# Optimization experiments

Hardware: AMD Instinct MI355X
Metric: run time of the kernel (lower is better)

The kernel has to match this reference:

```python
import jax, jax.numpy as jnp
import numpy as np

B, S, D_MODEL = 2, 2048, 1024
HEADS = 16
DK = D_MODEL // HEADS  # 64
Q_RANK, RANK = 6, 2
ROPE_BASE = 10000.0


def _xavier(key, shape):
    # torch nn.init.xavier_uniform_ on weight (out,in); stored here as (in,out)
    fan_in, fan_out = shape
    a = (6.0 / (fan_in + fan_out)) ** 0.5
    return jax.random.uniform(key, shape, jnp.float32, -a, a)


def setup_inputs() -> dict:
    key = jax.random.key(0)
    ks = jax.random.split(key, 10)
    inp = {
        "q": jax.random.normal(ks[0], (B, S, D_MODEL), jnp.float32),
        "k": jax.random.normal(ks[1], (B, S, D_MODEL), jnp.float32),
        "v": jax.random.normal(ks[2], (B, S, D_MODEL), jnp.float32),
        # causal mask; mask==0 -> -inf in scores
        "mask": jnp.tril(jnp.ones((S, S), dtype=bool))[None, None],
        "W_Aq": _xavier(ks[3], (D_MODEL, Q_RANK * HEADS)),
        "W_Ak": _xavier(ks[4], (D_MODEL, RANK * HEADS)),
        "W_Av": _xavier(ks[5], (D_MODEL, RANK * HEADS)),
        "W_Bq": _xavier(ks[6], (D_MODEL, Q_RANK * DK)),
        "W_Bk": _xavier(ks[7], (D_MODEL, RANK * DK)),
        "W_Bv": _xavier(ks[8], (D_MODEL, RANK * DK)),
        "Wo": _xavier(ks[9], (D_MODEL, D_MODEL)),
    }
    return inp


def _rotary_cos_sin(seq_len, dim):
    inv_freq = 1.0 / (ROPE_BASE ** (jnp.arange(0, dim, 2, dtype=jnp.float32) / dim))
    freqs = jnp.outer(jnp.arange(seq_len, dtype=jnp.float32), inv_freq)  # [S, dim/2]
    return jnp.cos(freqs)[None, :, None, :], jnp.sin(freqs)[None, :, None, :]


def _apply_rotary(x, cos, sin):
    # x: [B, S, R, dk]; rotate-half style RoPE
    d = x.shape[-1] // 2
    x1, x2 = x[..., :d], x[..., d:]
    return jnp.concatenate([x1 * cos + x2 * sin, -x1 * sin + x2 * cos], axis=-1)


def reference(q, k, v, mask, W_Aq, W_Ak, W_Av, W_Bq, W_Bk, W_Bv, Wo):
    Bn, Sn, D = q.shape
    # low-rank factor projections
    A_q = (q @ W_Aq).reshape(Bn, Sn, HEADS, Q_RANK)
    A_k = (k @ W_Ak).reshape(Bn, Sn, HEADS, RANK)
    A_v = (v @ W_Av).reshape(Bn, Sn, HEADS, RANK)
    B_q = (q @ W_Bq).reshape(Bn, Sn, Q_RANK, DK)
    B_k = (k @ W_Bk).reshape(Bn, Sn, RANK, DK)
    B_v = (v @ W_Bv).reshape(Bn, Sn, RANK, DK)
    cos, sin = _rotary_cos_sin(Sn, DK)
    B_q = _apply_rotary(B_q, cos, sin)
    B_k = _apply_rotary(B_k, cos, sin)
    # reconstruct per-head q/k/v: [B,H,S,dk]
    qh = jnp.einsum("bshr,bsrd->bhsd", A_q, B_q) / Q_RANK
    kh = jnp.einsum("bshr,bsrd->bhsd", A_k, B_k) / RANK
    vh = jnp.einsum("bshr,bsrd->bhsd", A_v, B_v) / RANK
    # NOTE: original divides by d_k (not sqrt(d_k)) -- faithful to source
    score = jnp.einsum("bhqd,bhkd->bhqk", qh, kh) / DK
    score = jnp.where(mask, score, -jnp.inf)
    # dropout is identity (eval / dropout=0.0)
    att = jax.nn.softmax(score, axis=-1)
    out = jnp.einsum("bhqk,bhkd->bqhd", att, vh).reshape(Bn, Sn, D)
    return out @ Wo
```

## Files before the change

### kernel.cpp

```cpp
#include <hip/hip_runtime.h>
#include <hip/hip_bf16.h>


typedef __attribute__((ext_vector_type(8))) short short8;
typedef __attribute__((ext_vector_type(4))) float floatx4;

#define MFMA16(a, b, c) __builtin_amdgcn_mfma_f32_16x16x32_bf16(a, b, c, 0, 0, 0)

__global__ __launch_bounds__(256) void cast3_kernel(const float* __restrict__ q,
                                                    const float* __restrict__ k,
                                                    const float* __restrict__ v,
                                                    __hip_bfloat16* __restrict__ qb,
                                                    __hip_bfloat16* __restrict__ kb,
                                                    __hip_bfloat16* __restrict__ vb) {
    const float* in = blockIdx.y == 0 ? q : blockIdx.y == 1 ? k : v;
    __hip_bfloat16* out = blockIdx.y == 0 ? qb : blockIdx.y == 1 ? kb : vb;
    int i = (blockIdx.x * 256 + threadIdx.x) * 4;
    float4 val = *(const float4*)(in + i);
    out[i + 0] = __float2bfloat16(val.x);
    out[i + 1] = __float2bfloat16(val.y);
    out[i + 2] = __float2bfloat16(val.z);
    out[i + 3] = __float2bfloat16(val.w);
}

__device__ __forceinline__ float wsrc(int n, int k,
                                      const float* __restrict__ Aq, const float* __restrict__ Bq,
                                      const float* __restrict__ Ak, const float* __restrict__ Bk,
                                      const float* __restrict__ Av, const float* __restrict__ Bv,
                                      const float* __restrict__ Wo) {
    if (n < 96) return Aq[(size_t)k * 96 + n];
    if (n < 480) return Bq[(size_t)k * 384 + (n - 96)];
    if (n < 512) return 0.f;
    if (n < 544) return Ak[(size_t)k * 32 + (n - 512)];
    if (n < 672) return Bk[(size_t)k * 128 + (n - 544)];
    if (n < 768) return 0.f;
    if (n < 800) return Av[(size_t)k * 32 + (n - 768)];
    if (n < 928) return Bv[(size_t)k * 128 + (n - 800)];
    if (n < 1024) return 0.f;
    return Wo[(size_t)k * 1024 + (n - 1024)];
}

__global__ __launch_bounds__(256) void pack_wT_kernel(const float* __restrict__ Aq,
                                                      const float* __restrict__ Bq,
                                                      const float* __restrict__ Ak,
                                                      const float* __restrict__ Bk,
                                                      const float* __restrict__ Av,
                                                      const float* __restrict__ Bv,
                                                      const float* __restrict__ Wo,
                                                      __hip_bfloat16* __restrict__ outBase) {
    __shared__ float tile[64][65];
    int k0 = blockIdx.x * 64, n0 = blockIdx.y * 64;
    int tid = threadIdx.x;
#pragma unroll
    for (int p = 0; p < 16; ++p) {
        int idx = p * 256 + tid;
        int kl = idx >> 6, nl = idx & 63;
        tile[kl][nl] = wsrc(n0 + nl, k0 + kl, Aq, Bq, Ak, Bk, Av, Bv, Wo);
    }
    __syncthreads();
#pragma unroll
    for (int p = 0; p < 16; ++p) {
        int idx = p * 256 + tid;
        int nl = idx >> 6, kl = idx & 63;
        outBase[(size_t)(n0 + nl) * 1024 + k0 + kl] = __float2bfloat16(tile[kl][nl]);
    }
}

__device__ __forceinline__ void gemm_body(const __hip_bfloat16* __restrict__ A,
                                          const __hip_bfloat16* __restrict__ BT,
                                          float* __restrict__ C, int N, int K,
                                          int m0, int n0) {
    __shared__ __align__(16) __hip_bfloat16 As[128][72];
    __shared__ __align__(16) __hip_bfloat16 Bs[128][72];
    int tid = threadIdx.x;
    int wave = tid >> 6, lane = tid & 63, quad = lane >> 4, l15 = lane & 15;
    int wm = wave >> 1, wn = wave & 1;
    floatx4 acc[4][4];
#pragma unroll
    for (int mt = 0; mt < 4; ++mt)
#pragma unroll
        for (int nt = 0; nt < 4; ++nt) acc[mt][nt] = (floatx4){0.f, 0.f, 0.f, 0.f};

    for (int k0 = 0; k0 < K; k0 += 64) {
#pragma unroll
        for (int p = 0; p < 4; ++p) {
            int idx = p * 256 + tid;
            int row = idx >> 3, c8 = (idx & 7) * 8;
            *(uint4*)&As[row][c8] = *(const uint4*)(A + (size_t)(m0 + row) * K + k0 + c8);
            *(uint4*)&Bs[row][c8] = *(const uint4*)(BT + (size_t)(n0 + row) * K + k0 + c8);
        }
        __syncthreads();
#pragma unroll
        for (int ks = 0; ks < 64; ks += 32) {
            short8 af[4], bf[4];
#pragma unroll
            for (int t = 0; t < 4; ++t) {
                af[t] = *(const short8*)&As[wm * 64 + t * 16 + l15][ks + quad * 8];
                bf[t] = *(const short8*)&Bs[wn * 64 + t * 16 + l15][ks + quad * 8];
            }
#pragma unroll
            for (int mt = 0; mt < 4; ++mt)
#pragma unroll
                for (int nt = 0; nt < 4; ++nt)
                    acc[mt][nt] = MFMA16(af[mt], bf[nt], acc[mt][nt]);
        }
        __syncthreads();
    }
#pragma unroll
    for (int mt = 0; mt < 4; ++mt)
#pragma unroll
        for (int nt = 0; nt < 4; ++nt)
#pragma unroll
            for (int r = 0; r < 4; ++r) {
                int row = m0 + wm * 64 + mt * 16 + quad * 4 + r;
                int col = n0 + wn * 64 + nt * 16 + l15;
                C[(size_t)row * N + col] = acc[mt][nt][r];
            }
}

__global__ __launch_bounds__(256) void gemm_bf16_kernel(const __hip_bfloat16* __restrict__ A,
                                                        const __hip_bfloat16* __restrict__ BT,
                                                        float* __restrict__ C, int N, int K) {
    gemm_body(A, BT, C, N, K, blockIdx.y * 128, blockIdx.x * 128);
}

__global__ __launch_bounds__(256) void gemm3_kernel(const __hip_bfloat16* __restrict__ qb,
                                                    const __hip_bfloat16* __restrict__ kb,
                                                    const __hip_bfloat16* __restrict__ vb,
                                                    const __hip_bfloat16* __restrict__ WqT,
                                                    const __hip_bfloat16* __restrict__ WkT,
                                                    const __hip_bfloat16* __restrict__ WvT,
                                                    float* __restrict__ Pq,
                                                    float* __restrict__ Pk,
                                                    float* __restrict__ Pv) {
    int t = blockIdx.x;
    const __hip_bfloat16* A; const __hip_bfloat16* BT; float* C; int N, nb;
    if (t < 4)      { A = qb; BT = WqT; C = Pq; N = 512; nb = t; }
    else if (t < 6) { A = kb; BT = WkT; C = Pk; N = 256; nb = t - 4; }
    else            { A = vb; BT = WvT; C = Pv; N = 256; nb = t - 6; }
    gemm_body(A, BT, C, N, 1024, blockIdx.y * 128, nb * 128);
}

__global__ __launch_bounds__(256) void combine_rope_kernel(const float* __restrict__ Pq,
                                                           const float* __restrict__ Pk,
                                                           const float* __restrict__ Pv,
                                                           __hip_bfloat16* __restrict__ qh,
                                                           __hip_bfloat16* __restrict__ kh,
                                                           __hip_bfloat16* __restrict__ vh) {
    int t = blockIdx.x, tid = threadIdx.x;
    int b = t >> 11, s = t & 2047;
    __shared__ float Lq[512], Lk[256], Lv[256];
    for (int i = tid; i < 512; i += 256) Lq[i] = Pq[(size_t)t * 512 + i];
    Lk[tid] = Pk[(size_t)t * 256 + tid];
    Lv[tid] = Pv[(size_t)t * 256 + tid];
    __syncthreads();
    if (tid < 192) {
        int r = tid >> 5, d = tid & 31;
        float inv = expf(-(float)d * 0.28782313662425576f);
        float sn, cs;
        sincosf((float)s * inv, &sn, &cs);
        float x1 = Lq[96 + r * 64 + d], x2 = Lq[96 + r * 64 + d + 32];
        Lq[96 + r * 64 + d] = x1 * cs + x2 * sn;
        Lq[96 + r * 64 + d + 32] = -x1 * sn + x2 * cs;
    } else {
        int i2 = tid - 192;
        int r = i2 >> 5, d = i2 & 31;
        float inv = expf(-(float)d * 0.28782313662425576f);
        float sn, cs;
        sincosf((float)s * inv, &sn, &cs);
        float x1 = Lk[32 + r * 64 + d], x2 = Lk[32 + r * 64 + d + 32];
        Lk[32 + r * 64 + d] = x1 * cs + x2 * sn;
        Lk[32 + r * 64 + d + 32] = -x1 * sn + x2 * cs;
    }
    __syncthreads();
    const float QSCALE = 1.4426950408889634f / 768.0f;
    int bh0 = b * 16;
    for (int i = tid; i < 1024; i += 256) {
        int h = i >> 6, d = i & 63;
        float aq = 0.f;
#pragma unroll
        for (int r = 0; r < 6; ++r) aq += Lq[h * 6 + r] * Lq[96 + r * 64 + d];
        size_t o = ((size_t)(bh0 + h) * 2048 + s) * 64 + d;
        qh[o] = __float2bfloat16(aq * QSCALE);
        float ak = Lk[h * 2] * Lk[32 + d] + Lk[h * 2 + 1] * Lk[96 + d];
        kh[o] = __float2bfloat16(ak);
        float av = Lv[h * 2] * Lv[32 + d] + Lv[h * 2 + 1] * Lv[96 + d];
        vh[o] = __float2bfloat16(av * 0.5f);
    }
}

__global__ __launch_bounds__(256) void transpose_v_kernel(const __hip_bfloat16* __restrict__ vh,
                                                          __hip_bfloat16* __restrict__ vT) {
    __shared__ __hip_bfloat16 tile[64][65];
    int s0 = blockIdx.x * 64, bh = blockIdx.y;
    int tid = threadIdx.x;
#pragma unroll
    for (int p = 0; p < 16; ++p) {
        int idx = p * 256 + tid;
        int r = idx >> 6, c = idx & 63;
        tile[r][c] = vh[((size_t)bh * 2048 + s0 + r) * 64 + c];
    }
    __syncthreads();
#pragma unroll
    for (int p = 0; p < 16; ++p) {
        int idx = p * 256 + tid;
        int r = idx >> 6, c = idx & 63;
        vT[((size_t)bh * 64 + r) * 2048 + s0 + c] = tile[c][r];
    }
}

__global__ __launch_bounds__(256) void flash_kernel(const __hip_bfloat16* __restrict__ qh,
                                                    const __hip_bfloat16* __restrict__ kh,
                                                    const __hip_bfloat16* __restrict__ vT,
                                                    __hip_bfloat16* __restrict__ att) {
    int lin = blockIdx.x + (blockIdx.y << 5);
    int bh = ((lin & 7) << 2) | ((lin >> 3) & 3);
    int qi = 31 - (lin >> 5);
    int tid = threadIdx.x;
    int wave = tid >> 6, lane = tid & 63, quad = lane >> 4, l15 = lane & 15;
    int q0 = qi * 64;
    __shared__ __align__(16) __hip_bfloat16 Ks[64][72];
    __shared__ __align__(16) __hip_bfloat16 Vts[64][72];
    __shared__ __align__(16) __hip_bfloat16 Ps[4][16][72];

    const __hip_bfloat16* qrow = qh + ((size_t)bh * 2048 + q0 + wave * 16 + l15) * 64 + quad * 8;
    short8 aq0 = *(const short8*)(qrow);
    short8 aq1 = *(const short8*)(qrow + 32);

    floatx4 o[4];
#pragma unroll
    for (int nt = 0; nt < 4; ++nt) o[nt] = (floatx4){0.f, 0.f, 0.f, 0.f};
    float rs[4] = {0.f, 0.f, 0.f, 0.f};

    for (int j = 0; j <= qi; ++j) {
        int k0 = j * 64;
#pragma unroll
        for (int p = 0; p < 2; ++p) {
            int idx = p * 256 + tid;
            int row = idx >> 3, c8 = (idx & 7) * 8;
            *(uint4*)&Ks[row][c8] = *(const uint4*)(kh + ((size_t)bh * 2048 + k0 + row) * 64 + c8);
            *(uint4*)&Vts[row][c8] = *(const uint4*)(vT + ((size_t)bh * 64 + row) * 2048 + k0 + c8);
        }
        __syncthreads();

        floatx4 s[4];
#pragma unroll
        for (int nt = 0; nt < 4; ++nt) s[nt] = (floatx4){0.f, 0.f, 0.f, 0.f};
#pragma unroll
        for (int nt = 0; nt < 4; ++nt) {
            short8 bk0 = *(const short8*)&Ks[nt * 16 + l15][quad * 8];
            short8 bk1 = *(const short8*)&Ks[nt * 16 + l15][32 + quad * 8];
            s[nt] = MFMA16(aq0, bk0, s[nt]);
            s[nt] = MFMA16(aq1, bk1, s[nt]);
        }
        if (j == qi) {
            int rbase = wave * 16 + quad * 4;
#pragma unroll
            for (int nt = 0; nt < 4; ++nt) {
                int cl = nt * 16 + l15;
#pragma unroll
                for (int r = 0; r < 4; ++r)
                    if (cl > rbase + r) s[nt][r] = -__builtin_inff();
            }
        }
        float pv[4][4];
#pragma unroll
        for (int nt = 0; nt < 4; ++nt)
#pragma unroll
            for (int r = 0; r < 4; ++r) {
                pv[nt][r] = exp2f(s[nt][r]);
                rs[r] += pv[nt][r];
            }
#pragma unroll
        for (int nt = 0; nt < 4; ++nt)
#pragma unroll
            for (int r = 0; r < 4; ++r)
                Ps[wave][quad * 4 + r][nt * 16 + l15] = __float2bfloat16(pv[nt][r]);
        __builtin_amdgcn_s_waitcnt(0xC07F);
        short8 pa0 = *(const short8*)&Ps[wave][l15][quad * 8];
        short8 pa1 = *(const short8*)&Ps[wave][l15][32 + quad * 8];
#pragma unroll
        for (int nt = 0; nt < 4; ++nt) {
            short8 bv0 = *(const short8*)&Vts[nt * 16 + l15][quad * 8];
            short8 bv1 = *(const short8*)&Vts[nt * 16 + l15][32 + quad * 8];
            o[nt] = MFMA16(pa0, bv0, o[nt]);
            o[nt] = MFMA16(pa1, bv1, o[nt]);
        }
        __syncthreads();
    }
    float l_i[4];
#pragma unroll
    for (int r = 0; r < 4; ++r) {
        float x = rs[r];
        x += __shfl_xor(x, 1, 64);
        x += __shfl_xor(x, 2, 64);
        x += __shfl_xor(x, 4, 64);
        x += __shfl_xor(x, 8, 64);
        l_i[r] = x;
    }
    int b = bh >> 4, h = bh & 15;
    size_t obase = ((size_t)b * 2048 + q0 + wave * 16 + quad * 4) * 1024 + h * 64;
#pragma unroll
    for (int nt = 0; nt < 4; ++nt)
#pragma unroll
        for (int r = 0; r < 4; ++r)
            att[obase + (size_t)r * 1024 + nt * 16 + l15] = __float2bfloat16(o[nt][r] / l_i[r]);
}

extern "C" void kernel_launch(void* const* d_in, const int* in_sizes, int n_in,
                              void* d_out, int out_size, void* d_ws, size_t ws_size,
                              hipStream_t stream) {
    const float* q = (const float*)d_in[0];
    const float* k = (const float*)d_in[1];
    const float* v = (const float*)d_in[2];
    const float* W_Aq = (const float*)d_in[4];
    const float* W_Ak = (const float*)d_in[5];
    const float* W_Av = (const float*)d_in[6];
    const float* W_Bq = (const float*)d_in[7];
    const float* W_Bk = (const float*)d_in[8];
    const float* W_Bv = (const float*)d_in[9];
    const float* Wo = (const float*)d_in[10];
    float* out = (float*)d_out;

    char* w = (char*)d_ws;
    __hip_bfloat16* qb = (__hip_bfloat16*)(w + 0);
    __hip_bfloat16* kb = (__hip_bfloat16*)(w + 8388608);
    __hip_bfloat16* vb = (__hip_bfloat16*)(w + 16777216);
    __hip_bfloat16* WqT = (__hip_bfloat16*)(w + 25165824);
    __hip_bfloat16* WkT = (__hip_bfloat16*)(w + 26214400);
    __hip_bfloat16* WvT = (__hip_bfloat16*)(w + 26738688);
    __hip_bfloat16* WoT = (__hip_bfloat16*)(w + 27262976);
    float* Pq = (float*)(w + 29360128);
    float* Pk = (float*)(w + 37748736);
    float* Pv = (float*)(w + 41943040);
    __hip_bfloat16* qh = qb;
    __hip_bfloat16* khp = kb;
    __hip_bfloat16* vhN = vb;
    __hip_bfloat16* att = (__hip_bfloat16*)(w + 29360128);
    __hip_bfloat16* vT = (__hip_bfloat16*)(w + 37748736);

    cast3_kernel<<<dim3(4096, 3), 256, 0, stream>>>(q, k, v, qb, kb, vb);
    pack_wT_kernel<<<dim3(16, 32), 256, 0, stream>>>(W_Aq, W_Bq, W_Ak, W_Bk, W_Av, W_Bv, Wo, WqT);
    gemm3_kernel<<<dim3(8, 32), 256, 0, stream>>>(qb, kb, vb, WqT, WkT, WvT, Pq, Pk, Pv);
    combine_rope_kernel<<<4096, 256, 0, stream>>>(Pq, Pk, Pv, qh, khp, vhN);
    transpose_v_kernel<<<dim3(32, 32), 256, 0, stream>>>(vhN, vT);
    flash_kernel<<<dim3(32, 32), 256, 0, stream>>>(qh, khp, vT, att);
    gemm_bf16_kernel<<<dim3(8, 32), 256, 0, stream>>>(att, WoT, out, 1024, 1024);
}
```

Before: 256.7 us.

## Fuse input cast into projection GEMM, enlarge flash tiles, narrow GEMM N-tiles

Removes the separate fp32-to-bf16 cast kernel by converting q/k/v to bf16 inside the projection GEMM's shared-memory load. The projection and output GEMMs switch to 128x64 tiles, which doubles the block count for better CU occupancy on a small grid. The flash kernel now processes 128 query rows per block (32 per wave), so each K/V tile load is reused across twice as many queries, and fully masked sub-tiles are skipped. RoPE sin/cos now use hardware sin/cos builtins on a range-reduced argument, which may cost accuracy for large positions.

```diff
diff --git a/kernel.cpp b/kernel.cpp
--- a/kernel.cpp
+++ b/kernel.cpp
@@ -7,20 +7,9 @@
 
 #define MFMA16(a, b, c) __builtin_amdgcn_mfma_f32_16x16x32_bf16(a, b, c, 0, 0, 0)
 
-__global__ __launch_bounds__(256) void cast3_kernel(const float* __restrict__ q,
-                                                    const float* __restrict__ k,
-                                                    const float* __restrict__ v,
-                                                    __hip_bfloat16* __restrict__ qb,
-                                                    __hip_bfloat16* __restrict__ kb,
-                                                    __hip_bfloat16* __restrict__ vb) {
-    const float* in = blockIdx.y == 0 ? q : blockIdx.y == 1 ? k : v;
-    __hip_bfloat16* out = blockIdx.y == 0 ? qb : blockIdx.y == 1 ? kb : vb;
-    int i = (blockIdx.x * 256 + threadIdx.x) * 4;
-    float4 val = *(const float4*)(in + i);
-    out[i + 0] = __float2bfloat16(val.x);
-    out[i + 1] = __float2bfloat16(val.y);
-    out[i + 2] = __float2bfloat16(val.z);
-    out[i + 3] = __float2bfloat16(val.w);
+__device__ __forceinline__ unsigned short bfbits(float x) {
+    __hip_bfloat16 h = __float2bfloat16(x);
+    return *(unsigned short*)&h;
 }
 
 __device__ __forceinline__ float wsrc(int n, int k,
@@ -66,42 +55,60 @@
     }
 }
 
-__device__ __forceinline__ void gemm_body(const __hip_bfloat16* __restrict__ A,
-                                          const __hip_bfloat16* __restrict__ BT,
-                                          float* __restrict__ C, int N, int K,
-                                          int m0, int n0) {
+__global__ __launch_bounds__(256) void gemm3_kernel(const float* __restrict__ q,
+                                                    const float* __restrict__ k,
+                                                    const float* __restrict__ v,
+                                                    const __hip_bfloat16* __restrict__ WT,
+                                                    float* __restrict__ Pq,
+                                                    float* __restrict__ Pk,
+                                                    float* __restrict__ Pv) {
     __shared__ __align__(16) __hip_bfloat16 As[128][72];
-    __shared__ __align__(16) __hip_bfloat16 Bs[128][72];
+    __shared__ __align__(16) __hip_bfloat16 Bs[64][72];
+    int t = blockIdx.x;
+    const float* A; float* C; int N, n0, wrow;
+    if (t < 8)       { A = q; C = Pq; N = 512; n0 = t * 64;        wrow = t * 64; }
+    else if (t < 12) { A = k; C = Pk; N = 256; n0 = (t - 8) * 64;  wrow = 512 + (t - 8) * 64; }
+    else             { A = v; C = Pv; N = 256; n0 = (t - 12) * 64; wrow = 768 + (t - 12) * 64; }
+    int m0 = blockIdx.y * 128;
     int tid = threadIdx.x;
     int wave = tid >> 6, lane = tid & 63, quad = lane >> 4, l15 = lane & 15;
     int wm = wave >> 1, wn = wave & 1;
-    floatx4 acc[4][4];
+    floatx4 acc[4][2];
 #pragma unroll
     for (int mt = 0; mt < 4; ++mt)
 #pragma unroll
-        for (int nt = 0; nt < 4; ++nt) acc[mt][nt] = (floatx4){0.f, 0.f, 0.f, 0.f};
-
-    for (int k0 = 0; k0 < K; k0 += 64) {
-#pragma unroll
-        for (int p = 0; p < 4; ++p) {
-            int idx = p * 256 + tid;
+        for (int nt = 0; nt < 2; ++nt) acc[mt][nt] = (floatx4){0.f, 0.f, 0.f, 0.f};
+
+    for (int k0 = 0; k0 < 1024; k0 += 64) {
+#pragma unroll
+        for (int pp = 0; pp < 8; ++pp) {
+            int idx = pp * 256 + tid;
+            int row = idx >> 4, c4 = (idx & 15) * 4;
+            float4 av = *(const float4*)(A + (size_t)(m0 + row) * 1024 + k0 + c4);
+            ushort4 bv;
+            bv.x = bfbits(av.x); bv.y = bfbits(av.y); bv.z = bfbits(av.z); bv.w = bfbits(av.w);
+            *(ushort4*)&As[row][c4] = bv;
+        }
+#pragma unroll
+        for (int pp = 0; pp < 2; ++pp) {
+            int idx = pp * 256 + tid;
             int row = idx >> 3, c8 = (idx & 7) * 8;
-            *(uint4*)&As[row][c8] = *(const uint4*)(A + (size_t)(m0 + row) * K + k0 + c8);
-            *(uint4*)&Bs[row][c8] = *(const uint4*)(BT + (size_t)(n0 + row) * K + k0 + c8);
+            *(uint4*)&Bs[row][c8] = *(const uint4*)(WT + (size_t)(wrow + row) * 1024 + k0 + c8);
         }
         __syncthreads();
 #pragma unroll
         for (int ks = 0; ks < 64; ks += 32) {
-            short8 af[4], bf[4];
-#pragma unroll
-            for (int t = 0; t < 4; ++t) {
-                af[t] = *(const short8*)&As[wm * 64 + t * 16 + l15][ks + quad * 8];
-                bf[t] = *(const short8*)&Bs[wn * 64 + t * 16 + l15][ks + quad * 8];
-            }
+            short8 af[4], bf[2];
+#pragma unroll
+            for (int t2 = 0; t2 < 4; ++t2)
+                af[t2] = *(const short8*)&As[wm * 64 + t2 * 16 + l15][ks + quad * 8];
+#pragma unroll
+            for (int t2 = 0; t2 < 2; ++t2)
+                bf[t2] = *(const short8*)&Bs[wn * 32 + t2 * 16 + l15][ks + quad * 8];
 #pragma unroll
             for (int mt = 0; mt < 4; ++mt)
 #pragma unroll
-                for (int nt = 0; nt < 4; ++nt)
+                for (int nt = 0; nt < 2; ++nt)
                     acc[mt][nt] = MFMA16(af[mt], bf[nt], acc[mt][nt]);
         }
         __syncthreads();
@@ -109,36 +116,71 @@
 #pragma unroll
     for (int mt = 0; mt < 4; ++mt)
 #pragma unroll
-        for (int nt = 0; nt < 4; ++nt)
+        for (int nt = 0; nt < 2; ++nt)
 #pragma unroll
             for (int r = 0; r < 4; ++r) {
                 int row = m0 + wm * 64 + mt * 16 + quad * 4 + r;
-                int col = n0 + wn * 64 + nt * 16 + l15;
+                int col = n0 + wn * 32 + nt * 16 + l15;
                 C[(size_t)row * N + col] = acc[mt][nt][r];
             }
 }
 
-__global__ __launch_bounds__(256) void gemm_bf16_kernel(const __hip_bfloat16* __restrict__ A,
-                                                        const __hip_bfloat16* __restrict__ BT,
-                                                        float* __restrict__ C, int N, int K) {
-    gemm_body(A, BT, C, N, K, blockIdx.y * 128, blockIdx.x * 128);
-}
-
-__global__ __launch_bounds__(256) void gemm3_kernel(const __hip_bfloat16* __restrict__ qb,
-                                                    const __hip_bfloat16* __restrict__ kb,
-                                                    const __hip_bfloat16* __restrict__ vb,
-                                                    const __hip_bfloat16* __restrict__ WqT,
-                                                    const __hip_bfloat16* __restrict__ WkT,
-                                                    const __hip_bfloat16* __restrict__ WvT,
-                                                    float* __restrict__ Pq,
-                                                    float* __restrict__ Pk,
-                                                    float* __restrict__ Pv) {
-    int t = blockIdx.x;
-    const __hip_bfloat16* A; const __hip_bfloat16* BT; float* C; int N, nb;
-    if (t < 4)      { A = qb; BT = WqT; C = Pq; N = 512; nb = t; }
-    else if (t < 6) { A = kb; BT = WkT; C = Pk; N = 256; nb = t - 4; }
-    else            { A = vb; BT = WvT; C = Pv; N = 256; nb = t - 6; }
-    gemm_body(A, BT, C, N, 1024, blockIdx.y * 128, nb * 128);
+__global__ __launch_bounds__(256) void gemm_out_kernel(const __hip_bfloat16* __restrict__ A,
+                                                       const __hip_bfloat16* __restrict__ BT,
+                                                       float* __restrict__ C) {
+    __shared__ __align__(16) __hip_bfloat16 As[128][72];
+    __shared__ __align__(16) __hip_bfloat16 Bs[64][72];
+    int n0 = blockIdx.x * 64, m0 = blockIdx.y * 128;
+    int tid = threadIdx.x;
+    int wave = tid >> 6, lane = tid & 63, quad = lane >> 4, l15 = lane & 15;
+    int wm = wave >> 1, wn = wave & 1;
+    floatx4 acc[4][2];
+#pragma unroll
+    for (int mt = 0; mt < 4; ++mt)
+#pragma unroll
+        for (int nt = 0; nt < 2; ++nt) acc[mt][nt] = (floatx4){0.f, 0.f, 0.f, 0.f};
+
+    for (int k0 = 0; k0 < 1024; k0 += 64) {
+#pragma unroll
+        for (int pp = 0; pp < 4; ++pp) {
+            int idx = pp * 256 + tid;
+            int row = idx >> 3, c8 = (idx & 7) * 8;
+            *(uint4*)&As[row][c8] = *(const uint4*)(A + (size_t)(m0 + row) * 1024 + k0 + c8);
+        }
+#pragma unroll
+        for (int pp = 0; pp < 2; ++pp) {
+            int idx = pp * 256 + tid;
+            int row = idx >> 3, c8 = (idx & 7) * 8;
+            *(uint4*)&Bs[row][c8] = *(const uint4*)(BT + (size_t)(n0 + row) * 1024 + k0 + c8);
+        }
+        __syncthreads();
+#pragma unroll
+        for (int ks = 0; ks < 64; ks += 32) {
+            short8 af[4], bf[2];
+#pragma unroll
+            for (int t2 = 0; t2 < 4; ++t2)
+                af[t2] = *(const short8*)&As[wm * 64 + t2 * 16 + l15][ks + quad * 8];
+#pragma unroll
+            for (int t2 = 0; t2 < 2; ++t2)
+                bf[t2] = *(const short8*)&Bs[wn * 32 + t2 * 16 + l15][ks + quad * 8];
+#pragma unroll
+            for (int mt = 0; mt < 4; ++mt)
+#pragma unroll
+                for (int nt = 0; nt < 2; ++nt)
+                    acc[mt][nt] = MFMA16(af[mt], bf[nt], acc[mt][nt]);
+        }
+        __syncthreads();
+    }
+#pragma unroll
+    for (int mt = 0; mt < 4; ++mt)
+#pragma unroll
+        for (int nt = 0; nt < 2; ++nt)
+#pragma unroll
+            for (int r = 0; r < 4; ++r) {
+                int row = m0 + wm * 64 + mt * 16 + quad * 4 + r;
+                int col = n0 + wn * 32 + nt * 16 + l15;
+                C[(size_t)row * 1024 + col] = acc[mt][nt][r];
+            }
 }
 
 __global__ __launch_bounds__(256) void combine_rope_kernel(const float* __restrict__ Pq,
@@ -156,18 +198,22 @@
     __syncthreads();
     if (tid < 192) {
         int r = tid >> 5, d = tid & 31;
-        float inv = expf(-(float)d * 0.28782313662425576f);
-        float sn, cs;
-        sincosf((float)s * inv, &sn, &cs);
+        float inv = __expf(-(float)d * 0.28782313662425576f);
+        float rev = (float)s * inv * 0.15915494309189535f;
+        rev -= floorf(rev);
+        float sn = __builtin_amdgcn_sinf(rev);
+        float cs = __builtin_amdgcn_cosf(rev);
         float x1 = Lq[96 + r * 64 + d], x2 = Lq[96 + r * 64 + d + 32];
         Lq[96 + r * 64 + d] = x1 * cs + x2 * sn;
         Lq[96 + r * 64 + d + 32] = -x1 * sn + x2 * cs;
     } else {
         int i2 = tid - 192;
         int r = i2 >> 5, d = i2 & 31;
-        float inv = expf(-(float)d * 0.28782313662425576f);
-        float sn, cs;
-        sincosf((float)s * inv, &sn, &cs);
+        float inv = __expf(-(float)d * 0.28782313662425576f);
+        float rev = (float)s * inv * 0.15915494309189535f;
+        rev -= floorf(rev);
+        float sn = __builtin_amdgcn_sinf(rev);
+        float cs = __builtin_amdgcn_cosf(rev);
         float x1 = Lk[32 + r * 64 + d], x2 = Lk[32 + r * 64 + d + 32];
         Lk[32 + r * 64 + d] = x1 * cs + x2 * sn;
         Lk[32 + r * 64 + d + 32] = -x1 * sn + x2 * cs;
@@ -213,98 +259,132 @@
                                                     const __hip_bfloat16* __restrict__ kh,
                                                     const __hip_bfloat16* __restrict__ vT,
                                                     __hip_bfloat16* __restrict__ att) {
-    int lin = blockIdx.x + (blockIdx.y << 5);
+    int lin = blockIdx.x + (blockIdx.y << 4);
     int bh = ((lin & 7) << 2) | ((lin >> 3) & 3);
-    int qi = 31 - (lin >> 5);
+    int p = 15 - (lin >> 5);
     int tid = threadIdx.x;
     int wave = tid >> 6, lane = tid & 63, quad = lane >> 4, l15 = lane & 15;
-    int q0 = qi * 64;
+    int q0 = p * 128;
     __shared__ __align__(16) __hip_bfloat16 Ks[64][72];
     __shared__ __align__(16) __hip_bfloat16 Vts[64][72];
-    __shared__ __align__(16) __hip_bfloat16 Ps[4][16][72];
-
-    const __hip_bfloat16* qrow = qh + ((size_t)bh * 2048 + q0 + wave * 16 + l15) * 64 + quad * 8;
-    short8 aq0 = *(const short8*)(qrow);
-    short8 aq1 = *(const short8*)(qrow + 32);
-
-    floatx4 o[4];
-#pragma unroll
-    for (int nt = 0; nt < 4; ++nt) o[nt] = (floatx4){0.f, 0.f, 0.f, 0.f};
-    float rs[4] = {0.f, 0.f, 0.f, 0.f};
-
-    for (int j = 0; j <= qi; ++j) {
+    __shared__ __align__(16) __hip_bfloat16 Ps[4][32][72];
+
+    short8 aq[2][2];
+#pragma unroll
+    for (int m = 0; m < 2; ++m) {
+        const __hip_bfloat16* qrow =
+            qh + ((size_t)bh * 2048 + q0 + wave * 32 + m * 16 + l15) * 64 + quad * 8;
+        aq[m][0] = *(const short8*)(qrow);
+        aq[m][1] = *(const short8*)(qrow + 32);
+    }
+
+    floatx4 o[2][4];
+#pragma unroll
+    for (int m = 0; m < 2; ++m)
+#pragma unroll
+        for (int nt = 0; nt < 4; ++nt) o[m][nt] = (floatx4){0.f, 0.f, 0.f, 0.f};
+    float rs[2][4] = {{0.f, 0.f, 0.f, 0.f}, {0.f, 0.f, 0.f, 0.f}};
+
+    int jmax = 2 * p + 1;
+    for (int j = 0; j <= jmax; ++j) {
         int k0 = j * 64;
 #pragma unroll
-        for (int p = 0; p < 2; ++p) {
-            int idx = p * 256 + tid;
+        for (int pp = 0; pp < 2; ++pp) {
+            int idx = pp * 256 + tid;
             int row = idx >> 3, c8 = (idx & 7) * 8;
             *(uint4*)&Ks[row][c8] = *(const uint4*)(kh + ((size_t)bh * 2048 + k0 + row) * 64 + c8);
             *(uint4*)&Vts[row][c8] = *(const uint4*)(vT + ((size_t)bh * 64 + row) * 2048 + k0 + c8);
         }
         __syncthreads();
 
-        floatx4 s[4];
-#pragma unroll
-        for (int nt = 0; nt < 4; ++nt) s[nt] = (floatx4){0.f, 0.f, 0.f, 0.f};
+        int krel = j - 2 * p;
+        bool skip0 = (krel == 1) && (wave * 32 < 64);
+        bool skip1 = (krel == 1) && (wave * 32 + 16 < 64);
+
+        floatx4 s[2][4];
+#pragma unroll
+        for (int m = 0; m < 2; ++m)
+#pragma unroll
+            for (int nt = 0; nt < 4; ++nt) s[m][nt] = (floatx4){0.f, 0.f, 0.f, 0.f};
 #pragma unroll
         for (int nt = 0; nt < 4; ++nt) {
             short8 bk0 = *(const short8*)&Ks[nt * 16 + l15][quad * 8];
             short8 bk1 = *(const short8*)&Ks[nt * 16 + l15][32 + quad * 8];
-            s[nt] = MFMA16(aq0, bk0, s[nt]);
-            s[nt] = MFMA16(aq1, bk1, s[nt]);
-        }
-        if (j == qi) {
-            int rbase = wave * 16 + quad * 4;
-#pragma unroll
-            for (int nt = 0; nt < 4; ++nt) {
-                int cl = nt * 16 + l15;
-#pragma unroll
-                for (int r = 0; r < 4; ++r)
-                    if (cl > rbase + r) s[nt][r] = -__builtin_inff();
-            }
-        }
-        float pv[4][4];
-#pragma unroll
-        for (int nt = 0; nt < 4; ++nt)
-#pragma unroll
-            for (int r = 0; r < 4; ++r) {
-                pv[nt][r] = exp2f(s[nt][r]);
-                rs[r] += pv[nt][r];
-            }
-#pragma unroll
-        for (int nt = 0; nt < 4; ++nt)
-#pragma unroll
-            for (int r = 0; r < 4; ++r)
-                Ps[wave][quad * 4 + r][nt * 16 + l15] = __float2bfloat16(pv[nt][r]);
+            if (!skip0) {
+                s[0][nt] = MFMA16(aq[0][0], bk0, s[0][nt]);
+                s[0][nt] = MFMA16(aq[0][1], bk1, s[0][nt]);
+            }
+            if (!skip1) {
+                s[1][nt] = MFMA16(aq[1][0], bk0, s[1][nt]);
+                s[1][nt] = MFMA16(aq[1][1], bk1, s[1][nt]);
+            }
+        }
+#pragma unroll
+        for (int m = 0; m < 2; ++m) {
+            bool skip = m == 0 ? skip0 : skip1;
+            if (skip) continue;
+            int sbase = wave * 32 + m * 16;
+            bool domask = (krel >= 0) && (krel * 64 + 63 > sbase);
+            if (domask) {
+#pragma unroll
+                for (int nt = 0; nt < 4; ++nt) {
+                    int kcol = k0 + nt * 16 + l15;
+#pragma unroll
+                    for (int r = 0; r < 4; ++r)
+                        if (kcol > q0 + sbase + quad * 4 + r) s[m][nt][r] = -__builtin_inff();
+                }
+            }
+#pragma unroll
+            for (int nt = 0; nt < 4; ++nt)
+#pragma unroll
+                for (int r = 0; r < 4; ++r) {
+                    float pe = exp2f(s[m][nt][r]);
+                    rs[m][r] += pe;
+                    Ps[wave][m * 16 + quad * 4 + r][nt * 16 + l15] = __float2bfloat16(pe);
+                }
+        }
         __builtin_amdgcn_s_waitcnt(0xC07F);
-        short8 pa0 = *(const short8*)&Ps[wave][l15][quad * 8];
-        short8 pa1 = *(const short8*)&Ps[wave][l15][32 + quad * 8];
+        short8 pa[2][2];
+#pragma unroll
+        for (int m = 0; m < 2; ++m) {
+            pa[m][0] = *(const short8*)&Ps[wave][m * 16 + l15][quad * 8];
+            pa[m][1] = *(const short8*)&Ps[wave][m * 16 + l15][32 + quad * 8];
+        }
 #pragma unroll
         for (int nt = 0; nt < 4; ++nt) {
             short8 bv0 = *(const short8*)&Vts[nt * 16 + l15][quad * 8];
             short8 bv1 = *(const short8*)&Vts[nt * 16 + l15][32 + quad * 8];
-            o[nt] = MFMA16(pa0, bv0, o[nt]);
-            o[nt] = MFMA16(pa1, bv1, o[nt]);
-        }
-        __syncthreads();
-    }
-    float l_i[4];
-#pragma unroll
-    for (int r = 0; r < 4; ++r) {
-        float x = rs[r];
-        x += __shfl_xor(x, 1, 64);
-        x += __shfl_xor(x, 2, 64);
-        x += __shfl_xor(x, 4, 64);
-        x += __shfl_xor(x, 8, 64);
-        l_i[r] = x;
+            if (!skip0) {
+                o[0][nt] = MFMA16(pa[0][0], bv0, o[0][nt]);
+                o[0][nt] = MFMA16(pa[0][1], bv1, o[0][nt]);
+            }
+            if (!skip1) {
+                o[1][nt] = MFMA16(pa[1][0], bv0, o[1][nt]);
+                o[1][nt] = MFMA16(pa[1][1], bv1, o[1][nt]);
+            }
+        }
+        __syncthreads();
     }
     int b = bh >> 4, h = bh & 15;
-    size_t obase = ((size_t)b * 2048 + q0 + wave * 16 + quad * 4) * 1024 + h * 64;
-#pragma unroll
-    for (int nt = 0; nt < 4; ++nt)
-#pragma unroll
-        for (int r = 0; r < 4; ++r)
-            att[obase + (size_t)r * 1024 + nt * 16 + l15] = __float2bfloat16(o[nt][r] / l_i[r]);
+#pragma unroll
+    for (int m = 0; m < 2; ++m) {
+        float l_i[4];
+#pragma unroll
+        for (int r = 0; r < 4; ++r) {
+            float x = rs[m][r];
+            x += __shfl_xor(x, 1, 64);
+            x += __shfl_xor(x, 2, 64);
+            x += __shfl_xor(x, 4, 64);
+            x += __shfl_xor(x, 8, 64);
+            l_i[r] = x;
+        }
+        size_t obase = ((size_t)b * 2048 + q0 + wave * 32 + m * 16 + quad * 4) * 1024 + h * 64;
+#pragma unroll
+        for (int nt = 0; nt < 4; ++nt)
+#pragma unroll
+            for (int r = 0; r < 4; ++r)
+                att[obase + (size_t)r * 1024 + nt * 16 + l15] = __float2bfloat16(o[m][nt][r] / l_i[r]);
+    }
 }
 
 extern "C" void kernel_launch(void* const* d_in, const int* in_sizes, int n_in,
@@ -323,27 +403,21 @@
     float* out = (float*)d_out;
 
     char* w = (char*)d_ws;
-    __hip_bfloat16* qb = (__hip_bfloat16*)(w + 0);
-    __hip_bfloat16* kb = (__hip_bfloat16*)(w + 8388608);
-    __hip_bfloat16* vb = (__hip_bfloat16*)(w + 16777216);
-    __hip_bfloat16* WqT = (__hip_bfloat16*)(w + 25165824);
-    __hip_bfloat16* WkT = (__hip_bfloat16*)(w + 26214400);
-    __hip_bfloat16* WvT = (__hip_bfloat16*)(w + 26738688);
+    __hip_bfloat16* qh = (__hip_bfloat16*)(w + 0);
+    __hip_bfloat16* khp = (__hip_bfloat16*)(w + 8388608);
+    __hip_bfloat16* vhN = (__hip_bfloat16*)(w + 16777216);
+    __hip_bfloat16* WT = (__hip_bfloat16*)(w + 25165824);
     __hip_bfloat16* WoT = (__hip_bfloat16*)(w + 27262976);
     float* Pq = (float*)(w + 29360128);
     float* Pk = (float*)(w + 37748736);
     float* Pv = (float*)(w + 41943040);
-    __hip_bfloat16* qh = qb;
-    __hip_bfloat16* khp = kb;
-    __hip_bfloat16* vhN = vb;
     __hip_bfloat16* att = (__hip_bfloat16*)(w + 29360128);
     __hip_bfloat16* vT = (__hip_bfloat16*)(w + 37748736);
 
-    cast3_kernel<<<dim3(4096, 3), 256, 0, stream>>>(q, k, v, qb, kb, vb);
-    pack_wT_kernel<<<dim3(16, 32), 256, 0, stream>>>(W_Aq, W_Bq, W_Ak, W_Bk, W_Av, W_Bv, Wo, WqT);
-    gemm3_kernel<<<dim3(8, 32), 256, 0, stream>>>(qb, kb, vb, WqT, WkT, WvT, Pq, Pk, Pv);
+    pack_wT_kernel<<<dim3(16, 32), 256, 0, stream>>>(W_Aq, W_Bq, W_Ak, W_Bk, W_Av, W_Bv, Wo, WT);
+    gemm3_kernel<<<dim3(16, 32), 256, 0, stream>>>(q, k, v, WT, Pq, Pk, Pv);
     combine_rope_kernel<<<4096, 256, 0, stream>>>(Pq, Pk, Pv, qh, khp, vhN);
     transpose_v_kernel<<<dim3(32, 32), 256, 0, stream>>>(vhN, vT);
-    flash_kernel<<<dim3(32, 32), 256, 0, stream>>>(qh, khp, vT, att);
-    gemm_bf16_kernel<<<dim3(8, 32), 256, 0, stream>>>(att, WoT, out, 1024, 1024);
-}
+    flash_kernel<<<dim3(16, 32), 256, 0, stream>>>(qh, khp, vT, att);
+    gemm_out_kernel<<<dim3(16, 32), 256, 0, stream>>>(att, WoT, out);
+}
```

Result: no change. 260.0 us (+1.3%).
